# Kernel tuning notes

Hardware: AMD Instinct MI355X
Metric: run time of the kernel (lower is better)

Reference implementation:

```python
import jax, jax.numpy as jnp
import numpy as np

BITS = 4
MAXQ = 15           # 2**BITS - 1
PACK = 32 // BITS   # 8 nibbles per int32
GROUP = 128         # quantization group size along in_features


def _unpack_rows(packed, rows):
    """Unpack int32-packed 4-bit values along axis 0. packed: [Kp, N] -> [rows, N]."""
    shifts = jnp.arange(0, 32, BITS, dtype=jnp.int32)            # [PACK]
    u = (packed[:, None, :] >> shifts[None, :, None]) & MAXQ    # [Kp, PACK, N]
    return u.reshape(-1, packed.shape[1])[:rows]


def _unpack_cols(packed, cols):
    """Unpack int32-packed 4-bit values along axis 1. packed: [G, Np] -> [G, cols]."""
    shifts = jnp.arange(0, 32, BITS, dtype=jnp.int32)            # [PACK]
    u = (packed[:, :, None] >> shifts[None, None, :]) & MAXQ    # [G, Np, PACK]
    return u.reshape(packed.shape[0], -1)[:, :cols]


def setup_inputs() -> dict:
    key = jax.random.key(0)
    k1, k2, k3, k4, k5 = jax.random.split(key, 5)
    K, N = 4096, 11008
    x = jax.random.normal(k1, (4, 2048, K), dtype=jnp.float32)
    qweight = jax.random.randint(k2, (K // PACK, N), 0, 2**31 - 1, dtype=jnp.int32)
    scales = jax.random.uniform(k3, (K // GROUP, N), dtype=jnp.float32)
    qzeros = jax.random.randint(k4, (K // GROUP, (N + PACK - 1) // PACK), 0, 2**31 - 1, dtype=jnp.int32)
    bias = jax.random.normal(k5, (N,), dtype=jnp.float32)
    return {"x": x, "qweight": qweight, "scales": scales, "qzeros": qzeros, "bias": bias}


def reference(x, qweight, scales, qzeros, bias):
    K = x.shape[-1]
    N = scales.shape[1]
    qw = _unpack_rows(qweight, K)            # [K, N] int in [0, 15]
    qz = _unpack_cols(qzeros, N) + 1         # [G, N] int in [1, 16] (+1 per get_unpacked_params)
    s = jnp.repeat(scales, GROUP, axis=0)    # [K, N]  groupwise -> per-row
    z = jnp.repeat(qz, GROUP, axis=0)        # [K, N]
    W = (qw - z).astype(x.dtype) * s         # dequantized weight [K, N]
    out = jnp.matmul(x, W) + bias
    return out.astype(x.dtype)
```

## Files before the change

### kernel.cpp

```cpp
#include <hip/hip_runtime.h>
#include <hip/hip_bf16.h>
#include <stdint.h>

typedef __attribute__((ext_vector_type(4))) float f32x4;
typedef __attribute__((ext_vector_type(8))) short bf16x8;
typedef __attribute__((ext_vector_type(8))) unsigned short ushort8;
typedef __attribute__((ext_vector_type(4))) unsigned short ushort4v;

__device__ __forceinline__ unsigned short f2bf(float f) {
    union { float f; unsigned int u; } v; v.f = f;
    unsigned int u = v.u;
    u += 0x7FFFu + ((u >> 16) & 1u);
    return (unsigned short)(u >> 16);
}

__device__ __forceinline__ int swz(int row, int k) {
    return (row * 64 + k) ^ ((row & 7) << 3);
}

__device__ __forceinline__ void gld16(const void* g, void* l) {
    __builtin_amdgcn_global_load_lds(
        (const __attribute__((address_space(1))) unsigned int*)g,
        (__attribute__((address_space(3))) unsigned int*)l,
        16, 0, 0);
}

__global__ __launch_bounds__(256)
void cvt_x(const float* __restrict__ X, unsigned short* __restrict__ Xb, long long n8) {
    long long i0 = (long long)blockIdx.x * 256 + threadIdx.x;
    long long stride = (long long)gridDim.x * 256;
    for (long long i = i0; i < n8; i += stride) {
        const float4* p = reinterpret_cast<const float4*>(X + i * 8);
        float4 a = p[0], b = p[1];
        ushort8 o;
        o[0] = f2bf(a.x); o[1] = f2bf(a.y); o[2] = f2bf(a.z); o[3] = f2bf(a.w);
        o[4] = f2bf(b.x); o[5] = f2bf(b.y); o[6] = f2bf(b.z); o[7] = f2bf(b.w);
        *reinterpret_cast<ushort8*>(Xb + i * 8) = o;
    }
}

__global__ __launch_bounds__(256)
void deq_w(const int* __restrict__ QW, const float* __restrict__ SC,
           const int* __restrict__ QZ, unsigned short* __restrict__ WT,
           int N, int K) {
    const int ntiles = N >> 6;
    const int nb = blockIdx.x % ntiles;
    const int kb = blockIdx.x / ntiles;
    const int n0 = nb * 64, kp0 = kb * 64;
    const int t = threadIdx.x;
    #pragma unroll
    for (int w = 0; w < 16; ++w) {
        const int p = t + 256 * w;
        const int kpo = p & 63, ni = p >> 6;
        const int n = n0 + ni, kp = kp0 + kpo;
        const int g = kp >> 4;
        const float s = SC[(size_t)g * N + n];
        const int zq = ((QZ[(size_t)g * (N >> 3) + (n >> 3)] >> ((n & 7) * 4)) & 15) + 1;
        const float zb = -(float)zq * s;
        const unsigned int q = (unsigned int)QW[(size_t)kp * N + n];
        ushort8 o;
        #pragma unroll
        for (int j = 0; j < 8; ++j)
            o[j] = f2bf(fmaf((float)((q >> (4 * j)) & 15u), s, zb));
        *reinterpret_cast<ushort8*>(&WT[(size_t)n * K + kp * 8]) = o;
    }
}

template<int KC, int NC>
__global__ __launch_bounds__(512, 2)
void qgemm_256(const unsigned short* __restrict__ Xb, const unsigned short* __restrict__ WT,
               const float* __restrict__ BIAS, float* __restrict__ OUT, int M) {
    __shared__ __align__(16) unsigned short S[65536];

    int id = blockIdx.x;
    const int nwg = gridDim.x;
    if ((nwg & 7) == 0) id = (id & 7) * (nwg >> 3) + (id >> 3);

    constexpr int ntn = NC >> 8;
    const int bm = (id / ntn) << 8;
    const int bn = (id % ntn) << 8;
    const int tid = threadIdx.x;
    const int lane = tid & 63;
    const int wid = tid >> 6;
    const int wm = (wid >> 2) * 64;
    const int wn = (wid & 3) * 32;
    const int lr = lane & 15;
    const int lk = (lane >> 4) * 8;

    f32x4 acc[8][4] = {};
    constexpr int nk = KC >> 6;

    auto stage_half = [&](int buf, int t, int kind, int half) {
        const unsigned short* gb = (kind ? WT + (size_t)(bn + half * 128) * KC
                                         : Xb + (size_t)(bm + half * 128) * KC) + (size_t)t * 64;
        unsigned short* lb = S + (kind ? 32768 : 0) + buf * 16384 + half * 8192;
        #pragma unroll
        for (int r = 0; r < 2; ++r) {
            const int s = r * 512 + tid;
            const int row = s >> 3, c8 = s & 7;
            gld16(gb + (size_t)row * KC + ((c8 ^ (row & 7)) << 3), lb + s * 8);
        }
    };

    bf16x8 aL[4][2], aH[4][2], bL[2][2], bH[2][2];

    auto loadA = [&](bf16x8 (&dst)[4][2], const unsigned short* Sa, int rbase) {
        #pragma unroll
        for (int i = 0; i < 4; ++i)
            #pragma unroll
            for (int kk = 0; kk < 2; ++kk)
                dst[i][kk] = *reinterpret_cast<const bf16x8*>(&Sa[swz(rbase + i * 16 + lr, kk * 32 + lk)]);
    };
    auto loadB = [&](bf16x8 (&dst)[2][2], const unsigned short* Sb, int rbase) {
        #pragma unroll
        for (int j = 0; j < 2; ++j)
            #pragma unroll
            for (int kk = 0; kk < 2; ++kk)
                dst[j][kk] = *reinterpret_cast<const bf16x8*>(&Sb[swz(rbase + j * 16 + lr, kk * 32 + lk)]);
    };
    auto quad = [&](bf16x8 (&A)[4][2], bf16x8 (&B)[2][2], int mi0, int nj0) {
        __builtin_amdgcn_s_setprio(1);
        #pragma unroll
        for (int kk = 0; kk < 2; ++kk)
            #pragma unroll
            for (int i = 0; i < 4; ++i)
                #pragma unroll
                for (int j = 0; j < 2; ++j)
                    acc[mi0 + i][nj0 + j] = __builtin_amdgcn_mfma_f32_16x16x32_bf16(
                        A[i][kk], B[j][kk], acc[mi0 + i][nj0 + j], 0, 0, 0);
        __builtin_amdgcn_s_setprio(0);
    };

    stage_half(0, 0, 0, 0); stage_half(0, 0, 0, 1);
    stage_half(0, 0, 1, 0); stage_half(0, 0, 1, 1);
    stage_half(1, 1, 0, 0); stage_half(1, 1, 1, 1); stage_half(1, 1, 0, 1);
    asm volatile("s_waitcnt vmcnt(6)" ::: "memory");
    __builtin_amdgcn_s_barrier();

    for (int t = 0; t < nk; ++t) {
        const int c = t & 1;
        const unsigned short* Sa = S + c * 16384;
        const unsigned short* Sb = S + 32768 + c * 16384;

        if (t + 1 < nk) stage_half(c ^ 1, t + 1, 1, 0);
        loadA(aL, Sa, wm);
        loadB(bL, Sb, wn);
        __builtin_amdgcn_s_barrier();
        quad(aL, bL, 0, 0);
        __builtin_amdgcn_s_barrier();

        if (t + 2 < nk) stage_half(c, t + 2, 0, 0);
        loadB(bH, Sb, 128 + wn);
        __builtin_amdgcn_s_barrier();
        quad(aL, bH, 0, 2);
        __builtin_amdgcn_s_barrier();

        if (t + 2 < nk) stage_half(c, t + 2, 1, 1);
        loadA(aH, Sa, 128 + wm);
        __builtin_amdgcn_s_barrier();
        quad(aH, bL, 4, 0);
        __builtin_amdgcn_s_barrier();

        if (t + 2 < nk) {
            stage_half(c, t + 2, 0, 1);
            asm volatile("s_waitcnt vmcnt(6)" ::: "memory");
        } else {
            asm volatile("s_waitcnt vmcnt(0)" ::: "memory");
        }
        __builtin_amdgcn_s_barrier();
        quad(aH, bH, 4, 2);
        __builtin_amdgcn_s_barrier();
    }

    #pragma unroll
    for (int mi = 0; mi < 8; ++mi) {
        const int row = bm + wm + (mi & 3) * 16 + ((mi >> 2) ? 128 : 0) + (lane >> 4) * 4;
        #pragma unroll
        for (int nj = 0; nj < 4; ++nj) {
            const int col = bn + wn + (nj & 1) * 16 + ((nj >> 1) ? 128 : 0) + lr;
            const float b = BIAS[col];
            #pragma unroll
            for (int r = 0; r < 4; ++r)
                OUT[(size_t)(row + r) * NC + col] = acc[mi][nj][r] + b;
        }
    }
}

__global__ __launch_bounds__(256, 2)
void qgemm_ws(const unsigned short* __restrict__ Xb, const unsigned short* __restrict__ WT,
              const float* __restrict__ BIAS, float* __restrict__ OUT,
              int M, int N, int K) {
    __shared__ __align__(16) unsigned short As[2][128 * 64];
    __shared__ __align__(16) unsigned short Bs[2][128 * 64];

    const int ntn = N >> 7;
    const int bm = (blockIdx.x / ntn) * 128;
    const int bn = (blockIdx.x % ntn) * 128;
    const int tid = threadIdx.x;
    const int lane = tid & 63;
    const int wave = tid >> 6;
    const int wm = (wave >> 1) * 64, wn = (wave & 1) * 64;
    const int lr = lane & 15, lk = (lane >> 4) * 8;

    f32x4 acc[4][4] = {};
    const int nk = K >> 6;

    auto stage = [&](int buf, int t) {
        const int k0 = t * 64;
        #pragma unroll
        for (int p = 0; p < 4; ++p) {
            const int slot = p * 256 + tid;
            const int row = slot >> 3, c = slot & 7;
            const int gk = k0 + ((c ^ (row & 7)) << 3);
            gld16(Xb + (size_t)(bm + row) * K + gk, &As[buf][slot * 8]);
            gld16(WT + (size_t)(bn + row) * K + gk, &Bs[buf][slot * 8]);
        }
    };

    auto compute = [&](int buf) {
        #pragma unroll
        for (int kk = 0; kk < 2; ++kk) {
            bf16x8 af[4], bfr[4];
            #pragma unroll
            for (int i = 0; i < 4; ++i) {
                af[i]  = *reinterpret_cast<const bf16x8*>(&As[buf][swz(wm + i * 16 + lr, kk * 32 + lk)]);
                bfr[i] = *reinterpret_cast<const bf16x8*>(&Bs[buf][swz(wn + i * 16 + lr, kk * 32 + lk)]);
            }
            #pragma unroll
            for (int i = 0; i < 4; ++i)
                #pragma unroll
                for (int j = 0; j < 4; ++j)
                    acc[i][j] = __builtin_amdgcn_mfma_f32_16x16x32_bf16(af[i], bfr[j], acc[i][j], 0, 0, 0);
        }
    };

    stage(0, 0);
    __syncthreads();
    int cur = 0;
    for (int t = 0; t < nk; ++t) {
        if (t + 1 < nk) stage(cur ^ 1, t + 1);
        compute(cur);
        __syncthreads();
        cur ^= 1;
    }

    #pragma unroll
    for (int i = 0; i < 4; ++i) {
        #pragma unroll
        for (int j = 0; j < 4; ++j) {
            const int col = bn + wn + j * 16 + lr;
            const float b = BIAS[col];
            #pragma unroll
            for (int r = 0; r < 4; ++r) {
                const int row = bm + wm + i * 16 + (lane >> 4) * 4 + r;
                OUT[(size_t)row * N + col] = acc[i][j][r] + b;
            }
        }
    }
}

__global__ __launch_bounds__(256, 2)
void qgemm_fb(const float* __restrict__ X, const int* __restrict__ QW,
              const float* __restrict__ SC, const int* __restrict__ QZ,
              const float* __restrict__ BIAS, float* __restrict__ OUT,
              int M, int N, int K) {
    __shared__ __align__(16) unsigned short As[2][128 * 64];
    __shared__ __align__(16) unsigned short Bs[2][128 * 64];

    const int ntn = N / 128;
    const int bm = (blockIdx.x / ntn) * 128;
    const int bn = (blockIdx.x % ntn) * 128;
    const int tid  = threadIdx.x;
    const int lane = tid & 63;
    const int wave = tid >> 6;
    const int wm = (wave >> 1) * 64, wn = (wave & 1) * 64;
    const int lr = lane & 15, lk = (lane >> 4) * 8;
    const int a_c4 = tid & 15, a_r0 = tid >> 4;
    const int b_n  = tid & 127, b_k0 = tid >> 7;

    f32x4 acc[4][4] = {};
    float4 va[8];
    unsigned int wb[4];
    float sc_s = 0.f, sc_zb = 0.f;
    const int nk = K / 64;

    auto gload = [&](int t) {
        const int k0 = t * 64;
        #pragma unroll
        for (int p = 0; p < 8; ++p)
            va[p] = *reinterpret_cast<const float4*>(X + (size_t)(bm + a_r0 + p * 16) * K + k0 + a_c4 * 4);
        const int g  = k0 >> 7;
        const int gn = bn + b_n;
        sc_s = SC[(size_t)g * N + gn];
        const int zq = ((QZ[(size_t)g * (N >> 3) + (gn >> 3)] >> ((gn & 7) * 4)) & 15) + 1;
        sc_zb = -(float)zq * sc_s;
        #pragma unroll
        for (int p = 0; p < 4; ++p)
            wb[p] = (unsigned int)QW[(size_t)(t * 8 + b_k0 + p * 2) * N + gn];
    };

    auto lwrite = [&](int buf) {
        #pragma unroll
        for (int p = 0; p < 8; ++p) {
            const int row = a_r0 + p * 16;
            ushort4v b;
            b.x = f2bf(va[p].x); b.y = f2bf(va[p].y);
            b.z = f2bf(va[p].z); b.w = f2bf(va[p].w);
            *reinterpret_cast<ushort4v*>(&As[buf][swz(row, a_c4 * 4)]) = b;
        }
        #pragma unroll
        for (int p = 0; p < 4; ++p) {
            const int ko = b_k0 + p * 2;
            ushort8 o;
            #pragma unroll
            for (int j = 0; j < 8; ++j)
                o[j] = f2bf(fmaf((float)((wb[p] >> (4 * j)) & 15u), sc_s, sc_zb));
            *reinterpret_cast<ushort8*>(&Bs[buf][swz(b_n, ko * 8)]) = o;
        }
    };

    auto compute = [&](int buf) {
        #pragma unroll
        for (int kk = 0; kk < 2; ++kk) {
            bf16x8 af[4], bfr[4];
            #pragma unroll
            for (int i = 0; i < 4; ++i) {
                af[i]  = *reinterpret_cast<const bf16x8*>(&As[buf][swz(wm + i * 16 + lr, kk * 32 + lk)]);
                bfr[i] = *reinterpret_cast<const bf16x8*>(&Bs[buf][swz(wn + i * 16 + lr, kk * 32 + lk)]);
            }
            #pragma unroll
            for (int i = 0; i < 4; ++i)
                #pragma unroll
                for (int j = 0; j < 4; ++j)
                    acc[i][j] = __builtin_amdgcn_mfma_f32_16x16x32_bf16(af[i], bfr[j], acc[i][j], 0, 0, 0);
        }
    };

    gload(0); lwrite(0);
    __syncthreads();
    for (int t = 0; t < nk; ++t) {
        if (t + 1 < nk) gload(t + 1);
        compute(t & 1);
        if (t + 1 < nk) lwrite((t + 1) & 1);
        __syncthreads();
    }

    #pragma unroll
    for (int i = 0; i < 4; ++i) {
        #pragma unroll
        for (int j = 0; j < 4; ++j) {
            const int col = bn + wn + j * 16 + lr;
            const float b = BIAS[col];
            #pragma unroll
            for (int r = 0; r < 4; ++r) {
                const int row = bm + wm + i * 16 + (lane >> 4) * 4 + r;
                OUT[(size_t)row * N + col] = acc[i][j][r] + b;
            }
        }
    }
}

extern "C" void kernel_launch(void* const* d_in, const int* in_sizes, int n_in,
                              void* d_out, int out_size, void* d_ws, size_t ws_size,
                              hipStream_t stream) {
    const float* X    = (const float*)d_in[0];
    const int*   QW   = (const int*)d_in[1];
    const float* SC   = (const float*)d_in[2];
    const int*   QZ   = (const int*)d_in[3];
    const float* BIAS = (const float*)d_in[4];
    float* OUT = (float*)d_out;

    const int N = in_sizes[4];
    const long long qwsz = in_sizes[1];
    const int K = (int)(qwsz * 8 / N);
    const int M = in_sizes[0] / K;

    const size_t xb_bytes = (size_t)M * K * 2;
    const size_t wt_bytes = (size_t)N * K * 2;

    if (ws_size >= xb_bytes + wt_bytes) {
        unsigned short* Xb = (unsigned short*)d_ws;
        unsigned short* WT = Xb + (size_t)M * K;

        cvt_x<<<2048, 256, 0, stream>>>(X, Xb, (long long)M * K / 8);
        deq_w<<<(N >> 6) * (K / 512), 256, 0, stream>>>(QW, SC, QZ, WT, N, K);

        if (K == 4096 && N == 11008 && (M % 256) == 0) {
            qgemm_256<4096, 11008><<<(M / 256) * (11008 / 256), 512, 0, stream>>>(Xb, WT, BIAS, OUT, M);
        } else {
            qgemm_ws<<<(M / 128) * (N / 128), 256, 0, stream>>>(Xb, WT, BIAS, OUT, M, N, K);
        }
    } else {
        qgemm_fb<<<(M / 128) * (N / 128), 256, 0, stream>>>(X, QW, SC, QZ, BIAS, OUT, M, N, K);
    }
}
```

Measured before the change: 783.9 us.

## Halve barriers per k-tile and precompute LDS and global stage addresses

Each k-step of the main loop is cut from eight workgroup barriers to four. LDS fragment reads now go straight into the MFMA quads without a barrier between them, and the loop is unrolled by two so buffer pointers are constants. The global-load source pointers and the swizzled LDS offsets are computed once outside the loop instead of per stage, which removes per-iteration integer work. The cost is a tighter set of ordering assumptions between the asynchronous LDS writes and other waves' reads, which could become a race if the remaining waits are not enough.

After: 746.7 us. -4.7%, faster.

```diff
diff --git a/kernel.cpp b/kernel.cpp
--- a/kernel.cpp
+++ b/kernel.cpp
@@ -87,36 +87,45 @@
     const int lr = lane & 15;
     const int lk = (lane >> 4) * 8;
 
+    const int xr  = (lr & 7) << 3;
+    const int lo0 = lk ^ xr;
+    const int lo1 = (32 + lk) ^ xr;
+    const int lrow = lr * 64;
+
     f32x4 acc[8][4] = {};
     constexpr int nk = KC >> 6;
 
-    auto stage_half = [&](int buf, int t, int kind, int half) {
-        const unsigned short* gb = (kind ? WT + (size_t)(bn + half * 128) * KC
-                                         : Xb + (size_t)(bm + half * 128) * KC) + (size_t)t * 64;
-        unsigned short* lb = S + (kind ? 32768 : 0) + buf * 16384 + half * 8192;
-        #pragma unroll
-        for (int r = 0; r < 2; ++r) {
-            const int s = r * 512 + tid;
-            const int row = s >> 3, c8 = s & 7;
-            gld16(gb + (size_t)row * KC + ((c8 ^ (row & 7)) << 3), lb + s * 8);
-        }
+    const int srow = tid >> 3;
+    const int scol = ((tid & 7) ^ (srow & 7)) << 3;
+    const unsigned short* gA[2] = { Xb + (size_t)(bm + srow) * KC + scol,
+                                    Xb + (size_t)(bm + 128 + srow) * KC + scol };
+    const unsigned short* gB[2] = { WT + (size_t)(bn + srow) * KC + scol,
+                                    WT + (size_t)(bn + 128 + srow) * KC + scol };
+
+    auto stage = [&](int buf, int tt, int kind, int half) {
+        const unsigned short* g = (kind ? gB[half] : gA[half]) + (size_t)tt * 64;
+        unsigned short* lb = S + (kind ? 32768 : 0) + buf * 16384 + half * 8192 + tid * 8;
+        gld16(g, lb);
+        gld16(g + (size_t)64 * KC, lb + 4096);
     };
 
     bf16x8 aL[4][2], aH[4][2], bL[2][2], bH[2][2];
 
     auto loadA = [&](bf16x8 (&dst)[4][2], const unsigned short* Sa, int rbase) {
-        #pragma unroll
-        for (int i = 0; i < 4; ++i)
-            #pragma unroll
-            for (int kk = 0; kk < 2; ++kk)
-                dst[i][kk] = *reinterpret_cast<const bf16x8*>(&Sa[swz(rbase + i * 16 + lr, kk * 32 + lk)]);
+        const unsigned short* p = Sa + rbase * 64 + lrow;
+        #pragma unroll
+        for (int i = 0; i < 4; ++i) {
+            dst[i][0] = *reinterpret_cast<const bf16x8*>(p + i * 1024 + lo0);
+            dst[i][1] = *reinterpret_cast<const bf16x8*>(p + i * 1024 + lo1);
+        }
     };
     auto loadB = [&](bf16x8 (&dst)[2][2], const unsigned short* Sb, int rbase) {
-        #pragma unroll
-        for (int j = 0; j < 2; ++j)
-            #pragma unroll
-            for (int kk = 0; kk < 2; ++kk)
-                dst[j][kk] = *reinterpret_cast<const bf16x8*>(&Sb[swz(rbase + j * 16 + lr, kk * 32 + lk)]);
+        const unsigned short* p = Sb + rbase * 64 + lrow;
+        #pragma unroll
+        for (int j = 0; j < 2; ++j) {
+            dst[j][0] = *reinterpret_cast<const bf16x8*>(p + j * 1024 + lo0);
+            dst[j][1] = *reinterpret_cast<const bf16x8*>(p + j * 1024 + lo1);
+        }
     };
     auto quad = [&](bf16x8 (&A)[4][2], bf16x8 (&B)[2][2], int mi0, int nj0) {
         __builtin_amdgcn_s_setprio(1);
@@ -131,45 +140,46 @@
         __builtin_amdgcn_s_setprio(0);
     };
 
-    stage_half(0, 0, 0, 0); stage_half(0, 0, 0, 1);
-    stage_half(0, 0, 1, 0); stage_half(0, 0, 1, 1);
-    stage_half(1, 1, 0, 0); stage_half(1, 1, 1, 1); stage_half(1, 1, 0, 1);
+    const unsigned short* Sa0 = S;
+    const unsigned short* Sa1 = S + 16384;
+    const unsigned short* Sb0 = S + 32768;
+    const unsigned short* Sb1 = S + 49152;
+
+    stage(0, 0, 0, 0); stage(0, 0, 0, 1);
+    stage(0, 0, 1, 0); stage(0, 0, 1, 1);
+    stage(1, 1, 0, 0); stage(1, 1, 1, 1); stage(1, 1, 0, 1);
     asm volatile("s_waitcnt vmcnt(6)" ::: "memory");
-    __builtin_amdgcn_s_barrier();
-
-    for (int t = 0; t < nk; ++t) {
-        const int c = t & 1;
-        const unsigned short* Sa = S + c * 16384;
-        const unsigned short* Sb = S + 32768 + c * 16384;
-
-        if (t + 1 < nk) stage_half(c ^ 1, t + 1, 1, 0);
+
+    auto tile = [&](int t, int c, const unsigned short* Sa, const unsigned short* Sb) {
+        __builtin_amdgcn_s_barrier();
+        if (t + 1 < nk) stage(c ^ 1, t + 1, 1, 0);
         loadA(aL, Sa, wm);
         loadB(bL, Sb, wn);
+        quad(aL, bL, 0, 0);
+
         __builtin_amdgcn_s_barrier();
-        quad(aL, bL, 0, 0);
+        if (t + 2 < nk) stage(c, t + 2, 0, 0);
+        loadB(bH, Sb, 128 + wn);
+        quad(aL, bH, 0, 2);
+
         __builtin_amdgcn_s_barrier();
-
-        if (t + 2 < nk) stage_half(c, t + 2, 0, 0);
-        loadB(bH, Sb, 128 + wn);
+        if (t + 2 < nk) stage(c, t + 2, 1, 1);
+        loadA(aH, Sa, 128 + wm);
+        quad(aH, bL, 4, 0);
+
         __builtin_amdgcn_s_barrier();
-        quad(aL, bH, 0, 2);
-        __builtin_amdgcn_s_barrier();
-
-        if (t + 2 < nk) stage_half(c, t + 2, 1, 1);
-        loadA(aH, Sa, 128 + wm);
-        __builtin_amdgcn_s_barrier();
-        quad(aH, bL, 4, 0);
-        __builtin_amdgcn_s_barrier();
-
         if (t + 2 < nk) {
-            stage_half(c, t + 2, 0, 1);
+            stage(c, t + 2, 0, 1);
             asm volatile("s_waitcnt vmcnt(6)" ::: "memory");
         } else {
             asm volatile("s_waitcnt vmcnt(0)" ::: "memory");
         }
-        __builtin_amdgcn_s_barrier();
         quad(aH, bH, 4, 2);
-        __builtin_amdgcn_s_barrier();
+    };
+
+    for (int t = 0; t < nk; t += 2) {
+        tile(t,     0, Sa0, Sb0);
+        tile(t + 1, 1, Sa1, Sb1);
     }
 
     #pragma unroll
```
